# Performance work log

Hardware: AMD Instinct MI355X
Metric: run time of the kernel (lower is better)

Reference implementation:

```python
import jax, jax.numpy as jnp
import numpy as np

MAX_SEQ_LEN = 1000

def _ln(x, g, b, eps=1e-5):
    m = jnp.mean(x, -1, keepdims=True)
    v = jnp.var(x, -1, keepdims=True)
    return (x - m) * jax.lax.rsqrt(v + eps) * g + b

def _conv1d(x, k, b):
    # x [B,T,Cin], k [K,Cin,Cout], 'SAME' padding (odd kernel)
    return jax.lax.conv_general_dilated(x, k, (1,), 'SAME', dimension_numbers=('NWC', 'WIO', 'NWC')) + b

def _dwconv(x, w):
    # lightweight conv: softmax-normalized depthwise kernel, w [C,K]
    k = jnp.transpose(jax.nn.softmax(w, axis=1))[:, None, :]  # [K,1,C]
    return jax.lax.conv_general_dilated(x, k, (1,), 'SAME', dimension_numbers=('NWC', 'WIO', 'NWC'), feature_group_count=x.shape[-1])

def _conv2d(x, k, b):
    # x [B,H,W,Cin], k [kh,kw,Cin,Cout]
    return jax.lax.conv_general_dilated(x, k, (1, 1), 'SAME', dimension_numbers=('NHWC', 'HWIO', 'NHWC')) + b

def _lconv(x, mask, ln_g, ln_b, glu_w, glu_b, dw, out_w, out_b):
    # LConvBlock: LN -> GLU projection -> depthwise lightweight conv -> out proj -> residual, masked
    res = x
    h = _ln(x, ln_g, ln_b)
    h = h @ glu_w + glu_b
    a, g = jnp.split(h, 2, axis=-1)
    h = a * jax.nn.sigmoid(g)
    h = jnp.where(mask[..., None], 0.0, h)
    h = _dwconv(h, dw)
    h = h @ out_w + out_b
    h = h + res
    return jnp.where(mask[..., None], 0.0, h)

def _forward(content_embedding, speaker_embedding_B, rhythm_B, scaled_duration_outputs,
             in_w, in_b,
             lc0_ln_g, lc0_ln_b, lc0_glu_w, lc0_glu_b, lc0_dw, lc0_out_w, lc0_out_b,
             lc1_ln_g, lc1_ln_b, lc1_glu_w, lc1_glu_b, lc1_dw, lc1_out_w, lc1_out_b,
             p1_w, p1_b, p2_k, p2_b,
             cw_k, cw_b, cw_ln_g, cw_ln_b,
             mkb1_k, mkb1_b, mkb2_k, mkb2_b,
             lw_w, lw_b, ln_g, ln_b, text_mask):
    B, S, _ = content_embedding.shape
    spk = jnp.broadcast_to(speaker_embedding_B[:, None, :], (B, S, speaker_embedding_B.shape[-1]))
    x = jnp.concatenate([content_embedding, spk], -1) @ in_w + in_b
    # duration predictor
    V = _lconv(x, text_mask, lc0_ln_g, lc0_ln_b, lc0_glu_w, lc0_glu_b, lc0_dw, lc0_out_w, lc0_out_b)
    V = _lconv(V, text_mask, lc1_ln_g, lc1_ln_b, lc1_glu_w, lc1_glu_b, lc1_dw, lc1_out_w, lc1_out_b)
    D = jax.nn.softplus(V @ p1_w + p1_b)[..., 0]
    D = jnp.where(text_mask, 0.0, D)
    T = _conv1d(V, p2_k, p2_b)  # [B,S,upsampled_dim]
    # learnable upsampling
    pred_phoneme_len = scaled_duration_outputs.sum(-1)
    alpha_B = jax.lax.stop_gradient(pred_phoneme_len / rhythm_B) / D.sum(-1)
    sD = alpha_B[:, None] * D
    sV = alpha_B[:, None, None] * V
    sT = alpha_B[:, None, None] * T
    mel_len = jnp.clip(jnp.round(sD.sum(-1)).astype(jnp.int32), 1, MAX_SEQ_LEN)
    mel_mask = jnp.arange(MAX_SEQ_LEN)[None, :] >= mel_len[:, None]  # True = pad
    attn_mask = mel_mask[:, :, None] & text_mask[:, None, :]  # bmm(mel_mask, src_mask^T).bool()
    e_k = jnp.cumsum(sD, axis=1)
    s_k = e_k - sD
    t = jnp.arange(1, MAX_SEQ_LEN + 1, dtype=sD.dtype)[None, :, None]
    Sm = jnp.where(attn_mask, 0.0, t - s_k[:, None, :])
    Em = jnp.where(attn_mask, 0.0, e_k[:, None, :] - t)
    # conv_w block: conv1d -> relu -> LN
    Cv = _ln(jax.nn.relu(_conv1d(sV, cw_k, cw_b)), cw_ln_g, cw_ln_b)  # [B,S,CW]
    feat = jnp.concatenate([Sm[..., None], Em[..., None],
                            jnp.broadcast_to(Cv[:, None, :, :], (B, MAX_SEQ_LEN, S, Cv.shape[-1]))], -1)
    h = jax.nn.silu(_conv2d(feat, mkb1_k, mkb1_b))
    h = jax.nn.silu(_conv2d(h, mkb2_k, mkb2_b))
    Wsc = (h @ lw_w + lw_b)[..., 0]  # [B,mel,S]
    Wsc = jnp.where(attn_mask | text_mask[:, None, :], -jnp.inf, Wsc)
    Wmat = jax.nn.softmax(Wsc, axis=2)
    up = jnp.matmul(Wmat, sT)
    up = _ln(up, ln_g, ln_b)
    up = jnp.where(mel_mask[..., None], 0.0, up)
    return up, Wmat, alpha_B, mel_len, mel_mask

def setup_inputs() -> dict:
    key = jax.random.key(0)
    ks = iter(jax.random.split(key, 64))
    B, S, DC, DS, H, CW, MKB, K = 8, 256, 192, 64, 256, 16, 16, 3
    def w(shape, scale=0.02):
        return jax.random.normal(next(ks), shape, jnp.float32) * scale
    inp = {}
    inp['content_embedding'] = jax.random.normal(next(ks), (B, S, DC), jnp.float32)
    inp['speaker_embedding_B'] = jax.random.normal(next(ks), (B, DS), jnp.float32)
    inp['rhythm_B'] = 0.15 + 0.1 * jax.random.uniform(next(ks), (B,), jnp.float32)
    inp['scaled_duration_outputs'] = jax.random.uniform(next(ks), (B, S), jnp.float32)
    lens = jax.random.randint(next(ks), (B,), 200, S + 1)
    inp['text_mask'] = jnp.arange(S)[None, :] >= lens[:, None]
    inp['in_w'] = w((DC + DS, H)); inp['in_b'] = jnp.zeros((H,), jnp.float32)
    for i in range(2):
        inp[f'lc{i}_ln_g'] = jnp.ones((H,), jnp.float32); inp[f'lc{i}_ln_b'] = jnp.zeros((H,), jnp.float32)
        inp[f'lc{i}_glu_w'] = w((H, 2 * H)); inp[f'lc{i}_glu_b'] = jnp.zeros((2 * H,), jnp.float32)
        inp[f'lc{i}_dw'] = w((H, K), 1.0)
        inp[f'lc{i}_out_w'] = w((H, H)); inp[f'lc{i}_out_b'] = jnp.zeros((H,), jnp.float32)
    inp['p1_w'] = w((H, 1)); inp['p1_b'] = jnp.zeros((1,), jnp.float32)
    inp['p2_k'] = w((K, H, H)); inp['p2_b'] = jnp.zeros((H,), jnp.float32)
    inp['cw_k'] = w((K, H, CW)); inp['cw_b'] = jnp.zeros((CW,), jnp.float32)
    inp['cw_ln_g'] = jnp.ones((CW,), jnp.float32); inp['cw_ln_b'] = jnp.zeros((CW,), jnp.float32)
    inp['mkb1_k'] = w((K, K, CW + 2, MKB)); inp['mkb1_b'] = jnp.zeros((MKB,), jnp.float32)
    inp['mkb2_k'] = w((K, K, MKB, MKB)); inp['mkb2_b'] = jnp.zeros((MKB,), jnp.float32)
    inp['lw_w'] = w((MKB, 1)); inp['lw_b'] = jnp.zeros((1,), jnp.float32)
    inp['ln_g'] = jnp.ones((H,), jnp.float32); inp['ln_b'] = jnp.zeros((H,), jnp.float32)
    return inp

def reference(content_embedding, speaker_embedding_B, rhythm_B, scaled_duration_outputs,
              text_mask,
              in_w, in_b,
              lc0_ln_g, lc0_ln_b, lc0_glu_w, lc0_glu_b, lc0_dw, lc0_out_w, lc0_out_b,
              lc1_ln_g, lc1_ln_b, lc1_glu_w, lc1_glu_b, lc1_dw, lc1_out_w, lc1_out_b,
              p1_w, p1_b, p2_k, p2_b,
              cw_k, cw_b, cw_ln_g, cw_ln_b,
              mkb1_k, mkb1_b, mkb2_k, mkb2_b,
              lw_w, lw_b, ln_g, ln_b):
    return _forward(content_embedding, speaker_embedding_B, rhythm_B, scaled_duration_outputs,
                    in_w, in_b,
                    lc0_ln_g, lc0_ln_b, lc0_glu_w, lc0_glu_b, lc0_dw, lc0_out_w, lc0_out_b,
                    lc1_ln_g, lc1_ln_b, lc1_glu_w, lc1_glu_b, lc1_dw, lc1_out_w, lc1_out_b,
                    p1_w, p1_b, p2_k, p2_b,
                    cw_k, cw_b, cw_ln_g, cw_ln_b,
                    mkb1_k, mkb1_b, mkb2_k, mkb2_b,
                    lw_w, lw_b, ln_g, ln_b, text_mask)
```

## Files before the change

kernel.cpp:

```cpp
#include <hip/hip_runtime.h>
#include <math.h>

#define SS 256
#define HH 256
#define MLEN 1000
#define CWW 16
#define NOC 16
#define RB 24

typedef __attribute__((ext_vector_type(8))) short bfrag;
typedef __attribute__((ext_vector_type(4))) float ffrag;

#define WS_V2     1048576u
#define WS_STT    1835008u
#define WS_WB     2097152u
#define WS_CCV    2424832u
#define WS_SSV    2457600u
#define WS_CCI    2490368u
#define WS_SSI    2523136u
#define WS_CP     2555904u
#define WS_CV     2654208u
#define WS_EK     2686976u
#define WS_SK     2689024u
#define WS_ALPHA  2691072u
#define WS_MELI   2691080u
#define WS_TMASK  2691088u

#define PK_IN     0u
#define PK_GLU0   65536u
#define PK_GLU1   196608u
#define PK_OUT0   327680u
#define PK_OUT1   393216u
#define PK_P2     458752u

#define OUT_UP    0u
#define OUT_W     2048000u
#define OUT_ALPHA 4096000u
#define OUT_MLEN  4096008u
#define OUT_MMASK 4096016u

__device__ __forceinline__ unsigned bf16rne(float x){
  unsigned u=__float_as_uint(x);
  u += 0x7fffu + ((u>>16)&1u);
  return u;
}
__device__ __forceinline__ unsigned short bf16h(float x){ return (unsigned short)(bf16rne(x)>>16); }
__device__ __forceinline__ float bf2f(unsigned short u){ return __uint_as_float(((unsigned)u)<<16); }
__device__ __forceinline__ int cvtpk(float lo, float hi){
  int r;
  asm("v_cvt_pk_bf16_f32 %0, %1, %2" : "=v"(r) : "v"(lo), "v"(hi));
  return r;
}
__device__ __forceinline__ float fsig(float x){
  return __builtin_amdgcn_rcpf(1.0f+__expf(-x));
}
__device__ __forceinline__ unsigned frag_idx(int k,int n,int KT){
  return (unsigned)(((((n>>4)*KT+(k>>5))*64 + ((k>>3)&3)*16 + (n&15))<<3) + (k&7));
}

__global__ __launch_bounds__(256) void k_prepmask(const void* __restrict__ traw,
    const float* __restrict__ in_w,
    const float* __restrict__ g0, const float* __restrict__ g1,
    const float* __restrict__ o0, const float* __restrict__ o1,
    const float* __restrict__ p2k, float* __restrict__ ws){
  int tid=threadIdx.x;
  if(blockIdx.x==256){
    __shared__ int s_fu, s_ff, s_nz;
    const unsigned char* mb=(const unsigned char*)traw;
    const unsigned int*  mw=(const unsigned int*)traw;
    if(tid==0){s_fu=0;s_ff=0;s_nz=0;}
    __syncthreads();
    int fu=0,ff=0,nz=0;
    for(int w=tid;w<512;w+=256){
      unsigned int v=mw[w];
      if(v){ nz=1; if(v==0x3F800000u) ff=1; else if(v&0xFFFFFF00u) fu=1; }
    }
    if(fu) atomicOr(&s_fu,1);
    if(ff) atomicOr(&s_ff,1);
    if(nz) atomicOr(&s_nz,1);
    __syncthreads();
    int words = (s_ff || (!s_fu && s_nz));
    for(int i=tid;i<2048;i+=256){
      unsigned int v = words ? mw[i] : (unsigned int)mb[i];
      ws[WS_TMASK+i] = v ? 1.0f : 0.0f;
    }
    return;
  }
  unsigned short* wb=(unsigned short*)(ws+WS_WB);
  int gid=blockIdx.x*256+tid, stride=65536;
  for(int i=gid;i<65536;i+=stride){ int k=i>>8,n=i&255; wb[PK_IN  +frag_idx(k,n,8)]=bf16h(in_w[i]); }
  for(int i=gid;i<131072;i+=stride){ int k=i>>9,n=i&511; wb[PK_GLU0+frag_idx(k,n,8)]=bf16h(g0[i]); }
  for(int i=gid;i<131072;i+=stride){ int k=i>>9,n=i&511; wb[PK_GLU1+frag_idx(k,n,8)]=bf16h(g1[i]); }
  for(int i=gid;i<65536;i+=stride){ int k=i>>8,n=i&255; wb[PK_OUT0+frag_idx(k,n,8)]=bf16h(o0[i]); }
  for(int i=gid;i<65536;i+=stride){ int k=i>>8,n=i&255; wb[PK_OUT1+frag_idx(k,n,8)]=bf16h(o1[i]); }
  for(int i=gid;i<196608;i+=stride){ int k3=i>>16,r=i&65535,k=r>>8,n=r&255;
    wb[PK_P2+(unsigned)k3*65536u+frag_idx(k,n,8)]=bf16h(p2k[i]); }
}

__global__ __launch_bounds__(256) void k_front(
    const float* __restrict__ ce, const float* __restrict__ spk,
    const unsigned short* __restrict__ wb, const float* __restrict__ in_b,
    const float* __restrict__ g0b, const float* __restrict__ ln0g, const float* __restrict__ ln0b,
    const float* __restrict__ dw0, const float* __restrict__ o0b,
    const float* __restrict__ g1b, const float* __restrict__ ln1g, const float* __restrict__ ln1b,
    const float* __restrict__ dw1, const float* __restrict__ o1b,
    const float* __restrict__ tmask, float* __restrict__ V2){
  __shared__ unsigned short Abf[16][264];
  __shared__ unsigned short Hb[16][264];
  __shared__ float Xf[16][264];
  __shared__ float Vf[16][264];
  __shared__ float dws[2][3][256];
  __shared__ float tmL[20];
  int b=blockIdx.x>>5, tile=blockIdx.x&31, s0=tile*8, tid=threadIdx.x;
  int w=tid>>6, lane=tid&63, lq=lane>>4, lm=lane&15;
  {
    float d0=dw0[tid*3],d1=dw0[tid*3+1],d2=dw0[tid*3+2];
    float mx=fmaxf(d0,fmaxf(d1,d2));
    float e0=__expf(d0-mx),e1=__expf(d1-mx),e2=__expf(d2-mx);
    float inv=1.0f/(e0+e1+e2);
    dws[0][0][tid]=e0*inv; dws[0][1][tid]=e1*inv; dws[0][2][tid]=e2*inv;
    d0=dw1[tid*3];d1=dw1[tid*3+1];d2=dw1[tid*3+2];
    mx=fmaxf(d0,fmaxf(d1,d2));
    e0=__expf(d0-mx);e1=__expf(d1-mx);e2=__expf(d2-mx);
    inv=1.0f/(e0+e1+e2);
    dws[1][0][tid]=e0*inv; dws[1][1][tid]=e1*inv; dws[1][2][tid]=e2*inv;
  }
  if(tid<18){
    int sI=s0-2+tid;
    tmL[tid]=(sI>=0&&sI<256)? tmask[b*256+sI] : 1.0f;
  }
  for(int it=0;it<16;it++){
    float v=0.f;
    int sI=s0-2+it;
    if(it<12 && sI>=0 && sI<256){
      int m=b*256+sI;
      v=(tid<192)? ce[m*192+tid] : spk[b*64+tid-192];
    }
    Abf[it][tid]=bf16h(v);
  }
  __syncthreads();
  {
    ffrag acc[4];
    #pragma unroll
    for(int j=0;j<4;j++){acc[j][0]=0;acc[j][1]=0;acc[j][2]=0;acc[j][3]=0;}
    #pragma unroll
    for(int kt=0;kt<8;kt++){
      bfrag af=*(const bfrag*)&Abf[lm][kt*32+lq*8];
      #pragma unroll
      for(int j=0;j<4;j++){
        int nt=w*4+j;
        bfrag bf=*(const bfrag*)(wb+PK_IN+((((unsigned)(nt*8+kt))*64u+(unsigned)lane)<<3));
        acc[j]=__builtin_amdgcn_mfma_f32_16x16x32_bf16(af,bf,acc[j],0,0,0);
      }
    }
    #pragma unroll
    for(int j=0;j<4;j++){
      int n=w*64+j*16+lm;
      float bn=in_b[n];
      #pragma unroll
      for(int reg=0;reg<4;reg++) Xf[lq*4+reg][n]=acc[j][reg]+bn;
    }
  }
  __syncthreads();
  {
    int r=tid>>4, seg=tid&15;
    if(r<12){
      float s=0.f,q=0.f;
      #pragma unroll
      for(int j4=0;j4<4;j4++){
        float4 v=*(const float4*)&Xf[r][seg*16+j4*4];
        s+=v.x+v.y+v.z+v.w; q+=v.x*v.x+v.y*v.y+v.z*v.z+v.w*v.w;
      }
      s+=__shfl_xor(s,1); q+=__shfl_xor(q,1);
      s+=__shfl_xor(s,2); q+=__shfl_xor(q,2);
      s+=__shfl_xor(s,4); q+=__shfl_xor(q,4);
      s+=__shfl_xor(s,8); q+=__shfl_xor(q,8);
      float mean=s*(1.0f/256.0f), rstd=rsqrtf(q*(1.0f/256.0f)-mean*mean+1e-5f);
      #pragma unroll
      for(int j4=0;j4<4;j4++){
        int c=seg*16+j4*4;
        float4 v=*(const float4*)&Xf[r][c];
        int p0=cvtpk((v.x-mean)*rstd*ln0g[c+0]+ln0b[c+0],(v.y-mean)*rstd*ln0g[c+1]+ln0b[c+1]);
        int p1=cvtpk((v.z-mean)*rstd*ln0g[c+2]+ln0b[c+2],(v.w-mean)*rstd*ln0g[c+3]+ln0b[c+3]);
        *(uint2*)&Abf[r][c]=make_uint2((unsigned)p0,(unsigned)p1);
      }
    } else {
      #pragma unroll
      for(int j4=0;j4<4;j4++) *(uint2*)&Abf[r][seg*16+j4*4]=make_uint2(0,0);
    }
  }
  __syncthreads();
  {
    ffrag aa[4],ag[4];
    #pragma unroll
    for(int j=0;j<4;j++){aa[j][0]=0;aa[j][1]=0;aa[j][2]=0;aa[j][3]=0;
                         ag[j][0]=0;ag[j][1]=0;ag[j][2]=0;ag[j][3]=0;}
    #pragma unroll
    for(int kt=0;kt<8;kt++){
      bfrag af=*(const bfrag*)&Abf[lm][kt*32+lq*8];
      #pragma unroll
      for(int j=0;j<4;j++){
        int nta=w*4+j, ntg=nta+16;
        bfrag bfa=*(const bfrag*)(wb+PK_GLU0+((((unsigned)(nta*8+kt))*64u+(unsigned)lane)<<3));
        bfrag bfg=*(const bfrag*)(wb+PK_GLU0+((((unsigned)(ntg*8+kt))*64u+(unsigned)lane)<<3));
        aa[j]=__builtin_amdgcn_mfma_f32_16x16x32_bf16(af,bfa,aa[j],0,0,0);
        ag[j]=__builtin_amdgcn_mfma_f32_16x16x32_bf16(af,bfg,ag[j],0,0,0);
      }
    }
    __syncthreads();
    #pragma unroll
    for(int j=0;j<4;j++){
      int n=w*64+j*16+lm;
      float ba=g0b[n], bg=g0b[n+256];
      #pragma unroll
      for(int reg=0;reg<4;reg++){
        int row=lq*4+reg;
        float a=aa[j][reg]+ba, g=ag[j][reg]+bg;
        float hv=a*fsig(g);
        if(row>=12||tmL[row]!=0.0f) hv=0.0f;
        Hb[row][n]=bf16h(hv);
      }
    }
  }
  __syncthreads();
  {
    float w0=dws[0][0][tid],w1=dws[0][1][tid],w2=dws[0][2][tid];
    for(int r=0;r<10;r++){
      float a=w0*bf2f(Hb[r][tid])+w1*bf2f(Hb[r+1][tid])+w2*bf2f(Hb[r+2][tid]);
      Abf[r][tid]=bf16h(a);
    }
    for(int r=10;r<16;r++) Abf[r][tid]=0;
  }
  __syncthreads();
  {
    ffrag acc[4];
    #pragma unroll
    for(int j=0;j<4;j++){acc[j][0]=0;acc[j][1]=0;acc[j][2]=0;acc[j][3]=0;}
    #pragma unroll
    for(int kt=0;kt<8;kt++){
      bfrag af=*(const bfrag*)&Abf[lm][kt*32+lq*8];
      #pragma unroll
      for(int j=0;j<4;j++){
        int nt=w*4+j;
        bfrag bf=*(const bfrag*)(wb+PK_OUT0+((((unsigned)(nt*8+kt))*64u+(unsigned)lane)<<3));
        acc[j]=__builtin_amdgcn_mfma_f32_16x16x32_bf16(af,bf,acc[j],0,0,0);
      }
    }
    #pragma unroll
    for(int j=0;j<4;j++){
      int n=w*64+j*16+lm;
      float bn=o0b[n];
      #pragma unroll
      for(int reg=0;reg<4;reg++){
        int row=lq*4+reg;
        float v=(row<10 && tmL[row+1]==0.0f)? acc[j][reg]+bn+Xf[row+1][n] : 0.0f;
        Vf[row][n]=v;
      }
    }
  }
  __syncthreads();
  {
    int r=tid>>4, seg=tid&15;
    if(r<10){
      float s=0.f,q=0.f;
      #pragma unroll
      for(int j4=0;j4<4;j4++){
        float4 v=*(const float4*)&Vf[r][seg*16+j4*4];
        s+=v.x+v.y+v.z+v.w; q+=v.x*v.x+v.y*v.y+v.z*v.z+v.w*v.w;
      }
      s+=__shfl_xor(s,1); q+=__shfl_xor(q,1);
      s+=__shfl_xor(s,2); q+=__shfl_xor(q,2);
      s+=__shfl_xor(s,4); q+=__shfl_xor(q,4);
      s+=__shfl_xor(s,8); q+=__shfl_xor(q,8);
      float mean=s*(1.0f/256.0f), rstd=rsqrtf(q*(1.0f/256.0f)-mean*mean+1e-5f);
      #pragma unroll
      for(int j4=0;j4<4;j4++){
        int c=seg*16+j4*4;
        float4 v=*(const float4*)&Vf[r][c];
        int p0=cvtpk((v.x-mean)*rstd*ln1g[c+0]+ln1b[c+0],(v.y-mean)*rstd*ln1g[c+1]+ln1b[c+1]);
        int p1=cvtpk((v.z-mean)*rstd*ln1g[c+2]+ln1b[c+2],(v.w-mean)*rstd*ln1g[c+3]+ln1b[c+3]);
        *(uint2*)&Abf[r][c]=make_uint2((unsigned)p0,(unsigned)p1);
      }
    } else {
      #pragma unroll
      for(int j4=0;j4<4;j4++) *(uint2*)&Abf[r][seg*16+j4*4]=make_uint2(0,0);
    }
  }
  __syncthreads();
  {
    ffrag aa[4],ag[4];
    #pragma unroll
    for(int j=0;j<4;j++){aa[j][0]=0;aa[j][1]=0;aa[j][2]=0;aa[j][3]=0;
                         ag[j][0]=0;ag[j][1]=0;ag[j][2]=0;ag[j][3]=0;}
    #pragma unroll
    for(int kt=0;kt<8;kt++){
      bfrag af=*(const bfrag*)&Abf[lm][kt*32+lq*8];
      #pragma unroll
      for(int j=0;j<4;j++){
        int nta=w*4+j, ntg=nta+16;
        bfrag bfa=*(const bfrag*)(wb+PK_GLU1+((((unsigned)(nta*8+kt))*64u+(unsigned)lane)<<3));
        bfrag bfg=*(const bfrag*)(wb+PK_GLU1+((((unsigned)(ntg*8+kt))*64u+(unsigned)lane)<<3));
        aa[j]=__builtin_amdgcn_mfma_f32_16x16x32_bf16(af,bfa,aa[j],0,0,0);
        ag[j]=__builtin_amdgcn_mfma_f32_16x16x32_bf16(af,bfg,ag[j],0,0,0);
      }
    }
    __syncthreads();
    #pragma unroll
    for(int j=0;j<4;j++){
      int n=w*64+j*16+lm;
      float ba=g1b[n], bg=g1b[n+256];
      #pragma unroll
      for(int reg=0;reg<4;reg++){
        int row=lq*4+reg;
        float a=aa[j][reg]+ba, g=ag[j][reg]+bg;
        float hv=a*fsig(g);
        if(row>=10||tmL[row+1]!=0.0f) hv=0.0f;
        Hb[row][n]=bf16h(hv);
      }
    }
  }
  __syncthreads();
  {
    float w0=dws[1][0][tid],w1=dws[1][1][tid],w2=dws[1][2][tid];
    for(int r=0;r<8;r++){
      float a=w0*bf2f(Hb[r][tid])+w1*bf2f(Hb[r+1][tid])+w2*bf2f(Hb[r+2][tid]);
      Abf[r][tid]=bf16h(a);
    }
    for(int r=8;r<16;r++) Abf[r][tid]=0;
  }
  __syncthreads();
  {
    ffrag acc[4];
    #pragma unroll
    for(int j=0;j<4;j++){acc[j][0]=0;acc[j][1]=0;acc[j][2]=0;acc[j][3]=0;}
    #pragma unroll
    for(int kt=0;kt<8;kt++){
      bfrag af=*(const bfrag*)&Abf[lm][kt*32+lq*8];
      #pragma unroll
      for(int j=0;j<4;j++){
        int nt=w*4+j;
        bfrag bf=*(const bfrag*)(wb+PK_OUT1+((((unsigned)(nt*8+kt))*64u+(unsigned)lane)<<3));
        acc[j]=__builtin_amdgcn_mfma_f32_16x16x32_bf16(af,bf,acc[j],0,0,0);
      }
    }
    #pragma unroll
    for(int j=0;j<4;j++){
      int n=w*64+j*16+lm;
      float bn=o1b[n];
      #pragma unroll
      for(int reg=0;reg<4;reg++){
        int row=lq*4+reg;
        if(row<8){
          float v=(tmL[row+2]!=0.0f)? 0.0f : acc[j][reg]+bn+Vf[row+1][n];
          V2[(unsigned)(b*256+s0+row)*256u+n]=v;
        }
      }
    }
  }
}

__global__ __launch_bounds__(256) void k_dur(const float* __restrict__ V2, const float* __restrict__ p1w,
    const float* __restrict__ p1b, const float* __restrict__ sdo, const float* __restrict__ rhythm,
    float* __restrict__ ws, float* __restrict__ outp){
  __shared__ float p1[HH];
  __shared__ float sd[SS];
  __shared__ float red[16];
  int b=blockIdx.x, tid=threadIdx.x;
  int wid=tid>>6, lane=tid&63;
  p1[tid]=p1w[tid];
  __syncthreads();
  float accd=p1b[0];
  const float* row=V2+(unsigned)(b*SS+tid)*HH;
  for(int k=0;k<HH;k+=4){
    float4 v=*(const float4*)&row[k];
    accd+=v.x*p1[k]+v.y*p1[k+1]+v.z*p1[k+2]+v.w*p1[k+3];
  }
  float Dv=fmaxf(accd,0.0f)+log1pf(expf(-fabsf(accd)));
  if(ws[WS_TMASK+b*SS+tid]!=0.0f) Dv=0.0f;
  float sv=sdo[b*SS+tid];
  float a=Dv, c=sv;
  for(int off=32;off;off>>=1){ a+=__shfl_down(a,off); c+=__shfl_down(c,off); }
  if(lane==0){ red[wid]=a; red[wid+8]=c; }
  __syncthreads();
  float Dsum=red[0]+red[1]+red[2]+red[3];
  float pred=red[8]+red[9]+red[10]+red[11];
  float al=(pred/rhythm[b])/Dsum;
  float sDv=al*Dv;
  sd[tid]=sDv;
  __syncthreads();
  for(int off=1;off<SS;off<<=1){
    float t=(tid>=off)?sd[tid-off]:0.0f;
    __syncthreads();
    sd[tid]+=t;
    __syncthreads();
  }
  float ek=sd[tid], sk=ek-sDv;
  ws[WS_EK+b*SS+tid]=ek;
  ws[WS_SK+b*SS+tid]=sk;
  float melf=sd[SS-1];
  int mel=(int)rintf(melf); mel=mel<1?1:(mel>MLEN?MLEN:mel);
  if(tid==0){
    ws[WS_ALPHA+b]=al;
    ((int*)ws)[WS_MELI+b]=mel;
    outp[OUT_ALPHA+b]=al;
    outp[OUT_MLEN+b]=(float)mel;
  }
  for(int t=tid;t<MLEN;t+=SS) outp[OUT_MMASK+b*MLEN+t]=(t>=mel)?1.0f:0.0f;
}

__global__ __launch_bounds__(256) void k_post(const float* __restrict__ V2,
    const unsigned short* __restrict__ wbp2, const float* __restrict__ p2b,
    const float* __restrict__ cwk, const float* __restrict__ cwb,
    const float* __restrict__ cwg, const float* __restrict__ cwbe,
    const float* __restrict__ mkb1k, const float* __restrict__ mkb1b,
    float* __restrict__ ws){
  int bx=blockIdx.x, tid=threadIdx.x;
  if(bx<256){
    __shared__ unsigned short Abf[18][264];
    int m0=(bx>>1)*16, nh=bx&1, b=m0>>8, s0=m0&255;
    for(int it=0;it<18;it++){
      int sI=s0-1+it;
      float v=(sI>=0&&sI<256)? V2[(unsigned)(b*256+sI)*256u+tid] : 0.0f;
      Abf[it][tid]=bf16h(v);
    }
    __syncthreads();
    int w=tid>>6, lane=tid&63, lq=lane>>4, lm=lane&15;
    ffrag acc[2];
    #pragma unroll
    for(int tt=0;tt<2;tt++){ acc[tt][0]=0;acc[tt][1]=0;acc[tt][2]=0;acc[tt][3]=0; }
    for(int k3=0;k3<3;k3++){
      const unsigned short* wb3=wbp2+(unsigned)k3*65536u;
      #pragma unroll
      for(int kt=0;kt<8;kt++){
        bfrag af=*(const bfrag*)&Abf[lm+k3][kt*32+lq*8];
        #pragma unroll
        for(int tt=0;tt<2;tt++){
          int nt=nh*8+w*2+tt;
          bfrag bf=*(const bfrag*)(wb3+((((unsigned)(nt*8+kt))*64u+(unsigned)lane)<<3));
          acc[tt]=__builtin_amdgcn_mfma_f32_16x16x32_bf16(af,bf,acc[tt],0,0,0);
        }
      }
    }
    float al=ws[WS_ALPHA+b];
    unsigned short* stt=(unsigned short*)(ws+WS_STT);
    #pragma unroll
    for(int tt=0;tt<2;tt++){
      int n=nh*128+w*32+tt*16+lm;
      float bn=p2b[n];
      unsigned short o0=bf16h((acc[tt][0]+bn)*al);
      unsigned short o1=bf16h((acc[tt][1]+bn)*al);
      unsigned short o2=bf16h((acc[tt][2]+bn)*al);
      unsigned short o3=bf16h((acc[tt][3]+bn)*al);
      *(uint2*)&stt[((unsigned)(b*256+n)<<8)+(unsigned)(s0+lq*4)]=
        make_uint2((unsigned)o0|((unsigned)o1<<16),(unsigned)o2|((unsigned)o3<<16));
    }
  } else if(bx<384){
    __shared__ float Vt[18][SS];
    int bb=bx-256;
    int b=bb>>4, tile=bb&15;
    int sbase=tile*16;
    float al=ws[WS_ALPHA+b];
    for(int rr=0;rr<18;rr++){
      int s=sbase-1+rr;
      Vt[rr][tid]=(s>=0&&s<SS)?al*V2[(b*SS+s)*HH+tid]:0.0f;
    }
    __syncthreads();
    int sl=tid>>4, oc=tid&15;
    float a0=cwb[oc],a1=0.f,a2=0.f,a3=0.f;
    for(int k3=0;k3<3;k3++){
      const float* vp=&Vt[sl+k3][0];
      const float* wpp=cwk+(unsigned)k3*HH*CWW+oc;
      for(int c=0;c<HH;c+=4){
        a0+=vp[c+0]*wpp[(c+0)*CWW];
        a1+=vp[c+1]*wpp[(c+1)*CWW];
        a2+=vp[c+2]*wpp[(c+2)*CWW];
        a3+=vp[c+3]*wpp[(c+3)*CWW];
      }
    }
    float acc=fmaxf((a0+a1)+(a2+a3),0.0f);
    float ssum=acc, qsum=acc*acc;
    for(int off=8;off;off>>=1){ ssum+=__shfl_xor(ssum,off); qsum+=__shfl_xor(qsum,off); }
    float mean=ssum*(1.0f/CWW), var=qsum*(1.0f/CWW)-mean*mean;
    float cv=(acc-mean)*rsqrtf(var+1e-5f)*cwg[oc]+cwbe[oc];
    ws[WS_CV+(unsigned)(b*SS+sbase+sl)*CWW+oc]=cv;
  } else {
    __shared__ float CvL[258][17];
    __shared__ float k1c[3][3][CWW][NOC];
    __shared__ float kab[3][3][2][NOC];
    __shared__ float skE[258], ekE[258], fiE[258];
    int b=bx-384;
    for(int i=tid;i<3*3*CWW*NOC;i+=256){
      int oc=i&15, ic=(i>>4)&15, kk=i>>8;
      int kw=kk%3, kh=kk/3;
      k1c[kh][kw][ic][oc]=mkb1k[((kh*3+kw)*18+2+ic)*NOC+oc];
    }
    for(int i=tid;i<3*3*2*NOC;i+=256){
      int oc=i&15, ch=(i>>4)&1, kk=i>>5;
      int kw=kk%3, kh=kk/3;
      kab[kh][kw][ch][oc]=mkb1k[((kh*3+kw)*18+ch)*NOC+oc];
    }
    for(int i=tid;i<SS*CWW;i+=256) CvL[1+(i>>4)][i&15]=ws[WS_CV+(unsigned)b*SS*CWW+i];
    if(tid<CWW){ CvL[0][tid]=0.f; CvL[257][tid]=0.f; }
    if(tid<258){
      float sk=0.f, ek=0.f, fi=0.f;
      if(tid>=1 && tid<=SS){
        sk=ws[WS_SK+b*SS+tid-1];
        ek=ws[WS_EK+b*SS+tid-1];
        fi=(ws[WS_TMASK+b*SS+tid-1]!=0.0f)?0.0f:1.0f;
      }
      skE[tid]=sk; ekE[tid]=ek; fiE[tid]=fi;
    }
    __syncthreads();
    float* cpg=ws+WS_CP+(unsigned)b*3*SS*NOC;
    float ccv[16],ssv[16],cci[16],ssi[16];
    #pragma unroll
    for(int oc=0;oc<NOC;oc++){ float bb2=mkb1b[oc]; ccv[oc]=bb2; cci[oc]=bb2; ssv[oc]=0.f; ssi[oc]=0.f; }
    for(int dt=0;dt<3;dt++){
      float acc[NOC];
      #pragma unroll
      for(int oc=0;oc<NOC;oc++) acc[oc]=0.f;
      #pragma unroll
      for(int ds=0;ds<3;ds++){
        #pragma unroll
        for(int ic=0;ic<CWW;ic++){
          float v=CvL[tid+ds][ic];
          #pragma unroll
          for(int oc=0;oc<NOC;oc++) acc[oc]+=v*k1c[dt][ds][ic][oc];
        }
      }
      for(int oc=0;oc<NOC;oc++) cpg[(unsigned)(dt*SS+tid)*NOC+oc]=acc[oc];
      float va[16],vb[16],ia[16],ib2[16];
      #pragma unroll
      for(int oc=0;oc<NOC;oc++){ va[oc]=0.f; vb[oc]=0.f; ia[oc]=0.f; ib2[oc]=0.f; }
      #pragma unroll
      for(int ds=0;ds<3;ds++){
        int j=tid+ds;
        float inb=(j>=1&&j<=SS)?1.0f:0.0f;
        float fb=fiE[j];
        float skv=skE[j], ekv=ekE[j];
        #pragma unroll
        for(int oc=0;oc<NOC;oc++){
          float ka=kab[dt][ds][0][oc], kb=kab[dt][ds][1][oc];
          float d=ka-kb, e=kb*ekv-ka*skv;
          va[oc]+=inb*d; vb[oc]+=inb*e; ia[oc]+=fb*d; ib2[oc]+=fb*e;
        }
      }
      float dtf=(float)dt;
      #pragma unroll
      for(int oc=0;oc<NOC;oc++){
        ccv[oc]+=acc[oc]+vb[oc]+dtf*va[oc]; ssv[oc]+=va[oc];
        cci[oc]+=acc[oc]+ib2[oc]+dtf*ia[oc]; ssi[oc]+=ia[oc];
      }
    }
    unsigned base=(unsigned)(b*SS+tid)*16u;
    for(int oc=0;oc<NOC;oc++){
      ws[WS_CCV+base+oc]=ccv[oc];
      ws[WS_SSV+base+oc]=ssv[oc];
      ws[WS_CCI+base+oc]=cci[oc];
      ws[WS_SSI+base+oc]=ssi[oc];
    }
  }
}

__global__ __launch_bounds__(256,4) void k_stageB(
    const float* __restrict__ ws, const float* __restrict__ mkb1k, const float* __restrict__ mkb1b,
    const float* __restrict__ mkb2k, const float* __restrict__ mkb2b,
    const float* __restrict__ lww, const float* __restrict__ lwb,
    float* __restrict__ outp){
  __shared__ __align__(16) short ringh[3][258][RB];
  __shared__ float skL[258], ekL[258];
  __shared__ unsigned char finC[260];
  __shared__ __align__(16) float wscL[SS];
  __shared__ float red[16];
  int bx=blockIdx.x, b=bx/125, chunk=bx%125, t0=chunk*8, tid=threadIdx.x;
  int wid=tid>>6, lane=tid&63;
  int lq=lane>>4, lm=lane&15;
  if(tid<258){
    float sk=0.f, ek=0.f; unsigned char fin=0;
    if(tid>=1 && tid<=SS){
      sk=ws[WS_SK+b*SS+tid-1];
      ek=ws[WS_EK+b*SS+tid-1];
      fin=(ws[WS_TMASK+b*SS+tid-1]!=0.0f)?0:1;
    }
    skL[tid]=sk; ekL[tid]=ek; finC[tid]=fin;
  }
  if(tid<72){
    int sl=tid/24, rem=tid%24;
    int row=(rem<12)?0:257, c=(rem%12)*2;
    *(int*)&ringh[sl][row][c]=0;
  }
  int mel=((const int*)ws)[WS_MELI+b];
  __syncthreads();

  const float* cpb=ws+WS_CP+(unsigned)b*3*SS*NOC;

  unsigned offA[5]; int dtL[5];
  bfrag bfw[5];
  {
    #pragma unroll
    for(int i=0;i<5;i++){
      int g=4*i+lq;
      int dt,ds,hf;
      if(g<18){ dt=g/6; int rm=g-6*dt; ds=rm>>1; hf=rm&1; }
      else { dt=0; ds=0; hf=0; }
      int srow=wid*64+lm+ds;
      offA[i]=(unsigned)((srow*RB+8*hf)*2);
      dtL[i]=dt;
      int pk[4];
      if(g<18){
        #pragma unroll
        for(int j=0;j<4;j++){
          unsigned u0=bf16rne(mkb2k[(8*g+2*j)*NOC+lm]);
          unsigned u1=bf16rne(mkb2k[(8*g+2*j+1)*NOC+lm]);
          pk[j]=(int)((u0>>16)|(u1&0xffff0000u));
        }
      } else pk[0]=pk[1]=pk[2]=pk[3]=0;
      bfw[i]=__builtin_bit_cast(bfrag, make_int4(pk[0],pk[1],pk[2],pk[3]));
    }
  }
  float4 b2q=*(const float4*)&mkb2b[lq*4];
  float4 lw4=*(const float4*)&lww[lq*4];
  float lwb0=lwb[0];
  const char* ringB=(const char*)&ringh[0][0][0];

  bool pureV=(t0>=2)&&(t0<=990)&&(t0+9<mel);
  bool pureI=(t0>=3)&&(t0<=990)&&(t0-2>=mel);
  bool pure=pureV||pureI;
  float ccR[16], ssR[16];
  if(pure){
    const float* cc=ws+(pureV?WS_CCV:WS_CCI)+(unsigned)(b*SS+tid)*16u;
    const float* s2=ws+(pureV?WS_SSV:WS_SSI)+(unsigned)(b*SS+tid)*16u;
    #pragma unroll
    for(int q=0;q<4;q++){
      float4 c4=((const float4*)cc)[q];
      float4 s4=((const float4*)s2)[q];
      ccR[4*q+0]=c4.x; ccR[4*q+1]=c4.y; ccR[4*q+2]=c4.z; ccR[4*q+3]=c4.w;
      ssR[4*q+0]=s4.x; ssR[4*q+1]=s4.y; ssR[4*q+2]=s4.z; ssR[4*q+3]=s4.w;
    }
  }

  auto conv1fast=[&](int T){
    int slot=T%3;
    float Tf=(float)T;
    int pk[8];
    #pragma unroll
    for(int j=0;j<8;j++){
      float x0=fmaf(Tf,ssR[2*j+0],ccR[2*j+0]);
      float x1=fmaf(Tf,ssR[2*j+1],ccR[2*j+1]);
      pk[j]=cvtpk(x0*fsig(x0),x1*fsig(x1));
    }
    int4* dst=(int4*)&ringh[slot][tid+1][0];
    dst[0]=make_int4(pk[0],pk[1],pk[2],pk[3]);
    dst[1]=make_int4(pk[4],pk[5],pk[6],pk[7]);
  };

  auto conv1gen=[&](int T){
    int slot=((T%3)+3)%3;
    int4* dst=(int4*)&ringh[slot][tid+1][0];
    if((unsigned)T>=(unsigned)MLEN){
      dst[0]=make_int4(0,0,0,0);
      dst[1]=make_int4(0,0,0,0);
      return;
    }
    int s=tid;
    float acc[NOC];
    bool fv=(T>=1)&&(T<=998)&&(T+1<mel);
    bool fi=(T>=2)&&(T<=998)&&(T-1>=mel);
    if(fv||fi){
      const float* cc=ws+(fv?WS_CCV:WS_CCI)+(unsigned)(b*SS+s)*16u;
      const float* s2=ws+(fv?WS_SSV:WS_SSI)+(unsigned)(b*SS+s)*16u;
      float Tf=(float)T;
      #pragma unroll
      for(int q=0;q<4;q++){
        float4 c4=((const float4*)cc)[q];
        float4 s4=((const float4*)s2)[q];
        acc[4*q+0]=c4.x+Tf*s4.x; acc[4*q+1]=c4.y+Tf*s4.y;
        acc[4*q+2]=c4.z+Tf*s4.z; acc[4*q+3]=c4.w+Tf*s4.w;
      }
    } else {
      #pragma unroll
      for(int oc=0;oc<NOC;oc++) acc[oc]=mkb1b[oc];
      #pragma unroll
      for(int dt=0;dt<3;dt++){
        int tr=T+dt-1;
        if(tr<0||tr>=MLEN) continue;
        bool valid=(tr<mel);
        float tt=(float)(tr+1);
        float gg[3], hh[3];
        #pragma unroll
        for(int ds=0;ds<3;ds++){
          int j=s+ds;
          float f = valid ? ((j>=1&&j<=SS)?1.0f:0.0f) : (float)finC[j];
          gg[ds]=f*(tt-skL[j]);
          hh[ds]=f*(ekL[j]-tt);
        }
        const float* cpr=cpb+(unsigned)(dt*SS+s)*NOC;
        float4 c0=((const float4*)cpr)[0], c1=((const float4*)cpr)[1];
        float4 c2=((const float4*)cpr)[2], c3=((const float4*)cpr)[3];
        acc[0]+=c0.x; acc[1]+=c0.y; acc[2]+=c0.z; acc[3]+=c0.w;
        acc[4]+=c1.x; acc[5]+=c1.y; acc[6]+=c1.z; acc[7]+=c1.w;
        acc[8]+=c2.x; acc[9]+=c2.y; acc[10]+=c2.z; acc[11]+=c2.w;
        acc[12]+=c3.x; acc[13]+=c3.y; acc[14]+=c3.z; acc[15]+=c3.w;
        #pragma unroll
        for(int ds=0;ds<3;ds++){
          const float* kA=mkb1k+((dt*3+ds)*18+0)*NOC;
          const float* kB=mkb1k+((dt*3+ds)*18+1)*NOC;
          #pragma unroll
          for(int oc=0;oc<NOC;oc++) acc[oc]+=gg[ds]*kA[oc]+hh[ds]*kB[oc];
        }
      }
    }
    int pk[8];
    #pragma unroll
    for(int j=0;j<8;j++){
      float x0=acc[2*j], x1=acc[2*j+1];
      pk[j]=cvtpk(x0*fsig(x0),x1*fsig(x1));
    }
    dst[0]=make_int4(pk[0],pk[1],pk[2],pk[3]);
    dst[1]=make_int4(pk[4],pk[5],pk[6],pk[7]);
  };

  if(pure){ conv1fast(t0-1); conv1fast(t0); conv1fast(t0+1); }
  else    { conv1gen (t0-1); conv1gen (t0); conv1gen (t0+1); }
  __syncthreads();

  #pragma unroll 1
  for(int r=0;r<8;r++){
    int t=t0+r;
    int tmod=t%3;
    ffrag acc2[4];
    #pragma unroll
    for(int tt=0;tt<4;tt++){ acc2[tt][0]=b2q.x; acc2[tt][1]=b2q.y; acc2[tt][2]=b2q.z; acc2[tt][3]=b2q.w; }
    #pragma unroll
    for(int i=0;i<5;i++){
      int dt=dtL[i];
      int x=tmod+dt+2; x=(x>=3)?x-3:x; x=(x>=3)?x-3:x;
      const char* rp=ringB+(unsigned)x*(258u*RB*2u)+offA[i];
      #pragma unroll
      for(int tt=0;tt<4;tt++){
        bfrag a=*(const bfrag*)(rp+tt*(16*RB*2));
        acc2[tt]=__builtin_amdgcn_mfma_f32_16x16x32_bf16(bfw[i],a,acc2[tt],0,0,0);
      }
    }
    float esum=0.f;
    #pragma unroll
    for(int tt=0;tt<4;tt++){
      float pvs=acc2[tt][0]*fsig(acc2[tt][0])*lw4.x
               +acc2[tt][1]*fsig(acc2[tt][1])*lw4.y
               +acc2[tt][2]*fsig(acc2[tt][2])*lw4.z
               +acc2[tt][3]*fsig(acc2[tt][3])*lw4.w;
      pvs+=__shfl_xor(pvs,16);
      pvs+=__shfl_xor(pvs,32);
      int s=wid*64+tt*16+lm;
      float fm=(float)finC[1+s];
      float ev=fm*__expf(pvs+lwb0);
      if(lane<16) wscL[s]=ev;
      esum+=ev;
    }
    esum+=__shfl_xor(esum,1);
    esum+=__shfl_xor(esum,2);
    esum+=__shfl_xor(esum,4);
    esum+=__shfl_xor(esum,8);
    if(lane==0) red[wid]=esum;
    __syncthreads();
    if(r<7){ if(pure) conv1fast(t+2); else conv1gen(t+2); }
    float tot=red[0]+red[1]+red[2]+red[3];
    outp[OUT_W+(unsigned)(b*MLEN+t)*SS+tid]=wscL[tid]*__builtin_amdgcn_rcpf(tot);
    if(r<7) __syncthreads();
  }
}

__global__ __launch_bounds__(256) void k_up(const float* __restrict__ ws,
    const float* __restrict__ lng, const float* __restrict__ lnb, float* __restrict__ outp){
  __shared__ unsigned short Wbf[16][264];
  __shared__ float UpL[16][264];
  __shared__ float gb[2][256];
  int bx=blockIdx.x, b=bx/63, tile=bx%63, t0=tile*16, tid=threadIdx.x;
  gb[0][tid]=lng[tid]; gb[1][tid]=lnb[tid];
  for(int it=0;it<16;it++){
    int t=t0+it;
    float v=(t<MLEN)? outp[OUT_W+(unsigned)(b*MLEN+t)*256u+tid] : 0.0f;
    Wbf[it][tid]=bf16h(v);
  }
  int mel=((const int*)ws)[WS_MELI+b];
  __syncthreads();
  int w=tid>>6, lane=tid&63, lq=lane>>4, lm=lane&15;
  const unsigned short* stt=(const unsigned short*)(ws+WS_STT)+(unsigned)b*65536u;
  ffrag acc[4];
  #pragma unroll
  for(int tt=0;tt<4;tt++){ acc[tt][0]=0;acc[tt][1]=0;acc[tt][2]=0;acc[tt][3]=0; }
  #pragma unroll
  for(int kt=0;kt<8;kt++){
    bfrag af=*(const bfrag*)&Wbf[lm][kt*32+lq*8];
    #pragma unroll
    for(int tt=0;tt<4;tt++){
      int n=w*64+tt*16+lm;
      bfrag bf=*(const bfrag*)(stt+((unsigned)n<<8)+(unsigned)(kt*32+lq*8));
      acc[tt]=__builtin_amdgcn_mfma_f32_16x16x32_bf16(af,bf,acc[tt],0,0,0);
    }
  }
  #pragma unroll
  for(int tt=0;tt<4;tt++){
    #pragma unroll
    for(int reg=0;reg<4;reg++)
      UpL[lq*4+reg][w*64+tt*16+lm]=acc[tt][reg];
  }
  __syncthreads();
  int r=tid>>4, seg=tid&15;
  float s=0.f,q=0.f;
  #pragma unroll
  for(int j4=0;j4<4;j4++){
    float4 v=*(const float4*)&UpL[r][seg*16+j4*4];
    s+=v.x+v.y+v.z+v.w; q+=v.x*v.x+v.y*v.y+v.z*v.z+v.w*v.w;
  }
  s+=__shfl_xor(s,1); q+=__shfl_xor(q,1);
  s+=__shfl_xor(s,2); q+=__shfl_xor(q,2);
  s+=__shfl_xor(s,4); q+=__shfl_xor(q,4);
  s+=__shfl_xor(s,8); q+=__shfl_xor(q,8);
  float mean=s*(1.0f/256.0f), rstd=rsqrtf(q*(1.0f/256.0f)-mean*mean+1e-5f);
  int t=t0+r;
  if(t<MLEN){
    bool vld=(t<mel);
    #pragma unroll
    for(int j4=0;j4<4;j4++){
      int c=seg*16+j4*4;
      float4 v=*(const float4*)&UpL[r][c];
      float4 o;
      o.x=vld?((v.x-mean)*rstd*gb[0][c+0]+gb[1][c+0]):0.0f;
      o.y=vld?((v.y-mean)*rstd*gb[0][c+1]+gb[1][c+1]):0.0f;
      o.z=vld?((v.z-mean)*rstd*gb[0][c+2]+gb[1][c+2]):0.0f;
      o.w=vld?((v.w-mean)*rstd*gb[0][c+3]+gb[1][c+3]):0.0f;
      *(float4*)&outp[OUT_UP+(unsigned)(b*MLEN+t)*256u+c]=o;
    }
  }
}

extern "C" void kernel_launch(void* const* d_in, const int* in_sizes, int n_in,
                              void* d_out, int out_size, void* d_ws, size_t ws_size,
                              hipStream_t stream){
  const float* ce   =(const float*)d_in[0];
  const float* spk  =(const float*)d_in[1];
  const float* rhy  =(const float*)d_in[2];
  const float* sdo  =(const float*)d_in[3];
  const void*  tmr  =d_in[4];
  const float* in_w =(const float*)d_in[5];
  const float* in_b =(const float*)d_in[6];
  const float* l0lg =(const float*)d_in[7];
  const float* l0lb =(const float*)d_in[8];
  const float* l0gw =(const float*)d_in[9];
  const float* l0gb =(const float*)d_in[10];
  const float* l0dw =(const float*)d_in[11];
  const float* l0ow =(const float*)d_in[12];
  const float* l0ob =(const float*)d_in[13];
  const float* l1lg =(const float*)d_in[14];
  const float* l1lb =(const float*)d_in[15];
  const float* l1gw =(const float*)d_in[16];
  const float* l1gb =(const float*)d_in[17];
  const float* l1dw =(const float*)d_in[18];
  const float* l1ow =(const float*)d_in[19];
  const float* l1ob =(const float*)d_in[20];
  const float* p1w  =(const float*)d_in[21];
  const float* p1b  =(const float*)d_in[22];
  const float* p2k  =(const float*)d_in[23];
  const float* p2b  =(const float*)d_in[24];
  const float* cwk  =(const float*)d_in[25];
  const float* cwb  =(const float*)d_in[26];
  const float* cwg  =(const float*)d_in[27];
  const float* cwbe =(const float*)d_in[28];
  const float* m1k  =(const float*)d_in[29];
  const float* m1b  =(const float*)d_in[30];
  const float* m2k  =(const float*)d_in[31];
  const float* m2b  =(const float*)d_in[32];
  const float* lww  =(const float*)d_in[33];
  const float* lwbp =(const float*)d_in[34];
  const float* lng  =(const float*)d_in[35];
  const float* lnb  =(const float*)d_in[36];
  float* ws=(float*)d_ws;
  float* outp=(float*)d_out;
  const unsigned short* wbb=(const unsigned short*)(ws+WS_WB);

  k_prepmask<<<257,256,0,stream>>>(tmr, in_w, l0gw, l1gw, l0ow, l1ow, p2k, ws);
  k_front   <<<256,256,0,stream>>>(ce, spk, wbb, in_b,
                                   l0gb, l0lg, l0lb, l0dw, l0ob,
                                   l1gb, l1lg, l1lb, l1dw, l1ob,
                                   ws+WS_TMASK, ws+WS_V2);
  k_dur     <<<8,256,0,stream>>>(ws+WS_V2, p1w, p1b, sdo, rhy, ws, outp);
  k_post    <<<392,256,0,stream>>>(ws+WS_V2, wbb+PK_P2, p2b, cwk, cwb, cwg, cwbe, m1k, m1b, ws);
  k_stageB  <<<1000,256,0,stream>>>(ws, m1k, m1b, m2k, m2b, lww, lwbp, outp);
  k_up      <<<504,256,0,stream>>>(ws, lng, lnb, outp);
}
```

Measured before the change: 287.7 us.

## Make stageB ring buffers per-wave and defer softmax normalization to k_up

Result: slower. 350.7 us (+21.9%).

```diff
diff --git a/kernel.cpp b/kernel.cpp
--- a/kernel.cpp
+++ b/kernel.cpp
@@ -20,6 +20,7 @@
 #define WS_SSI    2523136u
 #define WS_CP     2555904u
 #define WS_CV     2654208u
+#define WS_PSUM   2654208u
 #define WS_EK     2686976u
 #define WS_SK     2689024u
 #define WS_ALPHA  2691072u
@@ -563,15 +564,13 @@
 }
 
 __global__ __launch_bounds__(256,4) void k_stageB(
-    const float* __restrict__ ws, const float* __restrict__ mkb1k, const float* __restrict__ mkb1b,
+    float* __restrict__ ws, const float* __restrict__ mkb1k, const float* __restrict__ mkb1b,
     const float* __restrict__ mkb2k, const float* __restrict__ mkb2b,
     const float* __restrict__ lww, const float* __restrict__ lwb,
     float* __restrict__ outp){
-  __shared__ __align__(16) short ringh[3][258][RB];
+  __shared__ __align__(16) short ringw[4][3][66][RB];
   __shared__ float skL[258], ekL[258];
   __shared__ unsigned char finC[260];
-  __shared__ __align__(16) float wscL[SS];
-  __shared__ float red[16];
   int bx=blockIdx.x, b=bx/125, chunk=bx%125, t0=chunk*8, tid=threadIdx.x;
   int wid=tid>>6, lane=tid&63;
   int lq=lane>>4, lm=lane&15;
@@ -584,11 +583,6 @@
     }
     skL[tid]=sk; ekL[tid]=ek; finC[tid]=fin;
   }
-  if(tid<72){
-    int sl=tid/24, rem=tid%24;
-    int row=(rem<12)?0:257, c=(rem%12)*2;
-    *(int*)&ringh[sl][row][c]=0;
-  }
   int mel=((const int*)ws)[WS_MELI+b];
   __syncthreads();
 
@@ -603,8 +597,7 @@
       int dt,ds,hf;
       if(g<18){ dt=g/6; int rm=g-6*dt; ds=rm>>1; hf=rm&1; }
       else { dt=0; ds=0; hf=0; }
-      int srow=wid*64+lm+ds;
-      offA[i]=(unsigned)((srow*RB+8*hf)*2);
+      offA[i]=(unsigned)(((lm+ds)*RB+8*hf)*2);
       dtL[i]=dt;
       int pk[4];
       if(g<18){
@@ -621,7 +614,6 @@
   float4 b2q=*(const float4*)&mkb2b[lq*4];
   float4 lw4=*(const float4*)&lww[lq*4];
   float lwb0=lwb[0];
-  const char* ringB=(const char*)&ringh[0][0][0];
 
   bool pureV=(t0>=2)&&(t0<=990)&&(t0+9<mel);
   bool pureI=(t0>=3)&&(t0<=990)&&(t0-2>=mel);
@@ -639,31 +631,7 @@
     }
   }
 
-  auto conv1fast=[&](int T){
-    int slot=T%3;
-    float Tf=(float)T;
-    int pk[8];
-    #pragma unroll
-    for(int j=0;j<8;j++){
-      float x0=fmaf(Tf,ssR[2*j+0],ccR[2*j+0]);
-      float x1=fmaf(Tf,ssR[2*j+1],ccR[2*j+1]);
-      pk[j]=cvtpk(x0*fsig(x0),x1*fsig(x1));
-    }
-    int4* dst=(int4*)&ringh[slot][tid+1][0];
-    dst[0]=make_int4(pk[0],pk[1],pk[2],pk[3]);
-    dst[1]=make_int4(pk[4],pk[5],pk[6],pk[7]);
-  };
-
-  auto conv1gen=[&](int T){
-    int slot=((T%3)+3)%3;
-    int4* dst=(int4*)&ringh[slot][tid+1][0];
-    if((unsigned)T>=(unsigned)MLEN){
-      dst[0]=make_int4(0,0,0,0);
-      dst[1]=make_int4(0,0,0,0);
-      return;
-    }
-    int s=tid;
-    float acc[NOC];
+  auto conv1acc=[&](int s,int T,float* acc){
     bool fv=(T>=1)&&(T<=998)&&(T+1<mel);
     bool fi=(T>=2)&&(T<=998)&&(T-1>=mel);
     if(fv||fi){
@@ -674,8 +642,8 @@
       for(int q=0;q<4;q++){
         float4 c4=((const float4*)cc)[q];
         float4 s4=((const float4*)s2)[q];
-        acc[4*q+0]=c4.x+Tf*s4.x; acc[4*q+1]=c4.y+Tf*s4.y;
-        acc[4*q+2]=c4.z+Tf*s4.z; acc[4*q+3]=c4.w+Tf*s4.w;
+        acc[4*q+0]=fmaf(Tf,s4.x,c4.x); acc[4*q+1]=fmaf(Tf,s4.y,c4.y);
+        acc[4*q+2]=fmaf(Tf,s4.z,c4.z); acc[4*q+3]=fmaf(Tf,s4.w,c4.w);
       }
     } else {
       #pragma unroll
@@ -685,14 +653,14 @@
         int tr=T+dt-1;
         if(tr<0||tr>=MLEN) continue;
         bool valid=(tr<mel);
-        float tt=(float)(tr+1);
+        float tt2=(float)(tr+1);
         float gg[3], hh[3];
         #pragma unroll
         for(int ds=0;ds<3;ds++){
           int j=s+ds;
           float f = valid ? ((j>=1&&j<=SS)?1.0f:0.0f) : (float)finC[j];
-          gg[ds]=f*(tt-skL[j]);
-          hh[ds]=f*(ekL[j]-tt);
+          gg[ds]=f*(tt2-skL[j]);
+          hh[ds]=f*(ekL[j]-tt2);
         }
         const float* cpr=cpb+(unsigned)(dt*SS+s)*NOC;
         float4 c0=((const float4*)cpr)[0], c1=((const float4*)cpr)[1];
@@ -710,19 +678,53 @@
         }
       }
     }
+  };
+
+  auto packwrite=[&](const float* acc, short* dst){
     int pk[8];
     #pragma unroll
     for(int j=0;j<8;j++){
       float x0=acc[2*j], x1=acc[2*j+1];
       pk[j]=cvtpk(x0*fsig(x0),x1*fsig(x1));
     }
-    dst[0]=make_int4(pk[0],pk[1],pk[2],pk[3]);
-    dst[1]=make_int4(pk[4],pk[5],pk[6],pk[7]);
+    ((int4*)dst)[0]=make_int4(pk[0],pk[1],pk[2],pk[3]);
+    ((int4*)dst)[1]=make_int4(pk[4],pk[5],pk[6],pk[7]);
   };
 
-  if(pure){ conv1fast(t0-1); conv1fast(t0); conv1fast(t0+1); }
-  else    { conv1gen (t0-1); conv1gen (t0); conv1gen (t0+1); }
-  __syncthreads();
+  bool hl=(lane==0)||(lane==63);
+  int hrow=(lane==0)?0:65;
+  int hs=(lane==0)?(wid*64-1):(wid*64+64);
+
+  auto produce=[&](int T){
+    int slot=((T%3)+3)%3;
+    short* own=&ringw[wid][slot][lane+1][0];
+    short* hdst=&ringw[wid][slot][hrow][0];
+    if((unsigned)T>=(unsigned)MLEN){
+      ((int4*)own)[0]=make_int4(0,0,0,0); ((int4*)own)[1]=make_int4(0,0,0,0);
+      if(hl){ ((int4*)hdst)[0]=make_int4(0,0,0,0); ((int4*)hdst)[1]=make_int4(0,0,0,0); }
+      return;
+    }
+    float acc[16];
+    if(pure){
+      float Tf=(float)T;
+      #pragma unroll
+      for(int j=0;j<16;j++) acc[j]=fmaf(Tf,ssR[j],ccR[j]);
+    } else conv1acc(tid,T,acc);
+    packwrite(acc,own);
+    if(hl){
+      if(hs>=0&&hs<SS){
+        float a2[16];
+        conv1acc(hs,T,a2);
+        packwrite(a2,hdst);
+      } else {
+        ((int4*)hdst)[0]=make_int4(0,0,0,0); ((int4*)hdst)[1]=make_int4(0,0,0,0);
+      }
+    }
+  };
+
+  produce(t0-1); produce(t0); produce(t0+1);
+
+  const char* wring=(const char*)&ringw[wid][0][0][0];
 
   #pragma unroll 1
   for(int r=0;r<8;r++){
@@ -735,7 +737,7 @@
     for(int i=0;i<5;i++){
       int dt=dtL[i];
       int x=tmod+dt+2; x=(x>=3)?x-3:x; x=(x>=3)?x-3:x;
-      const char* rp=ringB+(unsigned)x*(258u*RB*2u)+offA[i];
+      const char* rp=wring+(unsigned)x*(66u*RB*2u)+offA[i];
       #pragma unroll
       for(int tt=0;tt<4;tt++){
         bfrag a=*(const bfrag*)(rp+tt*(16*RB*2));
@@ -754,19 +756,15 @@
       int s=wid*64+tt*16+lm;
       float fm=(float)finC[1+s];
       float ev=fm*__expf(pvs+lwb0);
-      if(lane<16) wscL[s]=ev;
+      if(lq==0) outp[OUT_W+(unsigned)(b*MLEN+t)*SS+s]=ev;
       esum+=ev;
     }
     esum+=__shfl_xor(esum,1);
     esum+=__shfl_xor(esum,2);
     esum+=__shfl_xor(esum,4);
     esum+=__shfl_xor(esum,8);
-    if(lane==0) red[wid]=esum;
-    __syncthreads();
-    if(r<7){ if(pure) conv1fast(t+2); else conv1gen(t+2); }
-    float tot=red[0]+red[1]+red[2]+red[3];
-    outp[OUT_W+(unsigned)(b*MLEN+t)*SS+tid]=wscL[tid]*__builtin_amdgcn_rcpf(tot);
-    if(r<7) __syncthreads();
+    if(lane==0) ws[WS_PSUM+(unsigned)(b*MLEN+t)*4u+(unsigned)wid]=esum;
+    if(r<7) produce(t+2);
   }
 }
 
@@ -775,14 +773,29 @@
   __shared__ unsigned short Wbf[16][264];
   __shared__ float UpL[16][264];
   __shared__ float gb[2][256];
+  __shared__ float rs[16];
   int bx=blockIdx.x, b=bx/63, tile=bx%63, t0=tile*16, tid=threadIdx.x;
   gb[0][tid]=lng[tid]; gb[1][tid]=lnb[tid];
+  if(tid<16){
+    int t=t0+tid; float s=0.f;
+    if(t<MLEN){
+      const float* pp=ws+WS_PSUM+(unsigned)(b*MLEN+t)*4u;
+      s=(pp[0]+pp[1])+(pp[2]+pp[3]);
+    }
+    rs[tid]=(s>0.f)?(1.0f/s):0.0f;
+  }
+  int mel=((const int*)ws)[WS_MELI+b];
+  __syncthreads();
   for(int it=0;it<16;it++){
     int t=t0+it;
-    float v=(t<MLEN)? outp[OUT_W+(unsigned)(b*MLEN+t)*256u+tid] : 0.0f;
+    float v=0.f;
+    if(t<MLEN){
+      float e=outp[OUT_W+(unsigned)(b*MLEN+t)*256u+tid];
+      v=e*rs[it];
+      outp[OUT_W+(unsigned)(b*MLEN+t)*256u+tid]=v;
+    }
     Wbf[it][tid]=bf16h(v);
   }
-  int mel=((const int*)ws)[WS_MELI+b];
   __syncthreads();
   int w=tid>>6, lane=tid&63, lq=lane>>4, lm=lane&15;
   const unsigned short* stt=(const unsigned short*)(ws+WS_STT)+(unsigned)b*65536u;
```

## Defer softmax normalization to k_up and remove per-step barrier in stageB

Applied to the files above, without the earlier changes.

After: 303.4 us, median of 3. 1.05x slower.

```diff
diff --git a/kernel.cpp b/kernel.cpp
--- a/kernel.cpp
+++ b/kernel.cpp
@@ -6,7 +6,7 @@
 #define MLEN 1000
 #define CWW 16
 #define NOC 16
-#define RB 24
+#define RB 16
 
 typedef __attribute__((ext_vector_type(8))) short bfrag;
 typedef __attribute__((ext_vector_type(4))) float ffrag;
@@ -20,6 +20,7 @@
 #define WS_SSI    2523136u
 #define WS_CP     2555904u
 #define WS_CV     2654208u
+#define WS_PSUM   2654208u
 #define WS_EK     2686976u
 #define WS_SK     2689024u
 #define WS_ALPHA  2691072u
@@ -563,15 +564,13 @@
 }
 
 __global__ __launch_bounds__(256,4) void k_stageB(
-    const float* __restrict__ ws, const float* __restrict__ mkb1k, const float* __restrict__ mkb1b,
+    float* __restrict__ ws, const float* __restrict__ mkb1k, const float* __restrict__ mkb1b,
     const float* __restrict__ mkb2k, const float* __restrict__ mkb2b,
     const float* __restrict__ lww, const float* __restrict__ lwb,
     float* __restrict__ outp){
-  __shared__ __align__(16) short ringh[3][258][RB];
+  __shared__ __align__(16) short ringh[4][258][RB];
   __shared__ float skL[258], ekL[258];
   __shared__ unsigned char finC[260];
-  __shared__ __align__(16) float wscL[SS];
-  __shared__ float red[16];
   int bx=blockIdx.x, b=bx/125, chunk=bx%125, t0=chunk*8, tid=threadIdx.x;
   int wid=tid>>6, lane=tid&63;
   int lq=lane>>4, lm=lane&15;
@@ -584,9 +583,9 @@
     }
     skL[tid]=sk; ekL[tid]=ek; finC[tid]=fin;
   }
-  if(tid<72){
-    int sl=tid/24, rem=tid%24;
-    int row=(rem<12)?0:257, c=(rem%12)*2;
+  if(tid<64){
+    int sl=tid>>4, rem=tid&15;
+    int row=(rem<8)?0:257, c=(rem&7)*2;
     *(int*)&ringh[sl][row][c]=0;
   }
   int mel=((const int*)ws)[WS_MELI+b];
@@ -640,7 +639,7 @@
   }
 
   auto conv1fast=[&](int T){
-    int slot=T%3;
+    int slot=T&3;
     float Tf=(float)T;
     int pk[8];
     #pragma unroll
@@ -655,7 +654,7 @@
   };
 
   auto conv1gen=[&](int T){
-    int slot=((T%3)+3)%3;
+    int slot=((T%4)+4)%4;
     int4* dst=(int4*)&ringh[slot][tid+1][0];
     if((unsigned)T>=(unsigned)MLEN){
       dst[0]=make_int4(0,0,0,0);
@@ -727,14 +726,15 @@
   #pragma unroll 1
   for(int r=0;r<8;r++){
     int t=t0+r;
-    int tmod=t%3;
+    if(r<7){ if(pure) conv1fast(t+2); else conv1gen(t+2); }
+    int tmod=t&3;
     ffrag acc2[4];
     #pragma unroll
     for(int tt=0;tt<4;tt++){ acc2[tt][0]=b2q.x; acc2[tt][1]=b2q.y; acc2[tt][2]=b2q.z; acc2[tt][3]=b2q.w; }
     #pragma unroll
     for(int i=0;i<5;i++){
       int dt=dtL[i];
-      int x=tmod+dt+2; x=(x>=3)?x-3:x; x=(x>=3)?x-3:x;
+      int x=tmod+dt+3; x=(x>=4)?x-4:x; x=(x>=4)?x-4:x;
       const char* rp=ringB+(unsigned)x*(258u*RB*2u)+offA[i];
       #pragma unroll
       for(int tt=0;tt<4;tt++){
@@ -742,7 +742,7 @@
         acc2[tt]=__builtin_amdgcn_mfma_f32_16x16x32_bf16(bfw[i],a,acc2[tt],0,0,0);
       }
     }
-    float esum=0.f;
+    float esum=0.f, evk=0.f;
     #pragma unroll
     for(int tt=0;tt<4;tt++){
       float pvs=acc2[tt][0]*fsig(acc2[tt][0])*lw4.x
@@ -754,18 +754,15 @@
       int s=wid*64+tt*16+lm;
       float fm=(float)finC[1+s];
       float ev=fm*__expf(pvs+lwb0);
-      if(lane<16) wscL[s]=ev;
+      if(lq==tt) evk=ev;
       esum+=ev;
     }
+    outp[OUT_W+(unsigned)(b*MLEN+t)*SS+(unsigned)(wid*64+lane)]=evk;
     esum+=__shfl_xor(esum,1);
     esum+=__shfl_xor(esum,2);
     esum+=__shfl_xor(esum,4);
     esum+=__shfl_xor(esum,8);
-    if(lane==0) red[wid]=esum;
-    __syncthreads();
-    if(r<7){ if(pure) conv1fast(t+2); else conv1gen(t+2); }
-    float tot=red[0]+red[1]+red[2]+red[3];
-    outp[OUT_W+(unsigned)(b*MLEN+t)*SS+tid]=wscL[tid]*__builtin_amdgcn_rcpf(tot);
+    if(lane==0) ws[WS_PSUM+(unsigned)(b*MLEN+t)*4u+(unsigned)wid]=esum;
     if(r<7) __syncthreads();
   }
 }
@@ -775,14 +772,29 @@
   __shared__ unsigned short Wbf[16][264];
   __shared__ float UpL[16][264];
   __shared__ float gb[2][256];
+  __shared__ float rs[16];
   int bx=blockIdx.x, b=bx/63, tile=bx%63, t0=tile*16, tid=threadIdx.x;
   gb[0][tid]=lng[tid]; gb[1][tid]=lnb[tid];
+  if(tid<16){
+    int t=t0+tid; float s=0.f;
+    if(t<MLEN){
+      const float* pp=ws+WS_PSUM+(unsigned)(b*MLEN+t)*4u;
+      s=(pp[0]+pp[1])+(pp[2]+pp[3]);
+    }
+    rs[tid]=(s>0.f)?(1.0f/s):0.0f;
+  }
+  int mel=((const int*)ws)[WS_MELI+b];
+  __syncthreads();
   for(int it=0;it<16;it++){
     int t=t0+it;
-    float v=(t<MLEN)? outp[OUT_W+(unsigned)(b*MLEN+t)*256u+tid] : 0.0f;
+    float v=0.f;
+    if(t<MLEN){
+      float e=outp[OUT_W+(unsigned)(b*MLEN+t)*256u+tid];
+      v=e*rs[it];
+      outp[OUT_W+(unsigned)(b*MLEN+t)*256u+tid]=v;
+    }
     Wbf[it][tid]=bf16h(v);
   }
-  int mel=((const int*)ws)[WS_MELI+b];
   __syncthreads();
   int w=tid>>6, lane=tid&63, lq=lane>>4, lm=lane&15;
   const unsigned short* stt=(const unsigned short*)(ws+WS_STT)+(unsigned)b*65536u;
```
